# Performance work log

Hardware: AMD Instinct MI355X
Metric: run time of the kernel (lower is better)

Reference implementation:

```python
import jax, jax.numpy as jnp
import numpy as np

TAU = 2.0       # init_tau
VTH = 1.0       # v_threshold
VRESET = 0.0    # v_reset (hard reset)
ALPHA = 2.0     # ATan surrogate width
H = 8           # num_heads
W = 20          # attention_window
TIME_STEP = 2   # config.time_step -> global_scale uses 1000 // time_step


@jax.custom_vjp
def spike(x):
    return (x >= 0.0).astype(x.dtype)

def _spike_fwd(x):
    return (x >= 0.0).astype(x.dtype), x

def _spike_bwd(x, g):
    # ATan surrogate gradient (spikingjelly default)
    sg = (ALPHA / 2.0) / (1.0 + (jnp.pi / 2.0 * ALPHA * x) ** 2)
    return (g * sg,)

spike.defvjp(_spike_fwd, _spike_bwd)


def lif(x_seq):
    """Multi-step LIF, decay_input=False, hard reset. x_seq: [T, ...] -> spikes [T, ...]."""
    def step(v, x):
        h = v - (v - VRESET) / TAU + x          # neuronal charge (decay_input=False)
        s = spike(h - VTH)
        v_new = s * VRESET + (1.0 - s) * h      # hard reset
        return v_new, s
    _, s_seq = jax.lax.scan(step, jnp.zeros_like(x_seq[0]), x_seq)
    return s_seq


def bn(x, gamma, beta, eps=1e-5):
    # BatchNorm1d step_mode='m': stats over (T, B) per channel (training-mode stats)
    mean = x.mean(axis=(0, 1))
    var = x.var(axis=(0, 1))
    return (x - mean) * jax.lax.rsqrt(var + eps) * gamma + beta


def _shift(a, o):
    # a: [B, H, T, D]; out[..., t, :] = a[..., t + o, :], zero outside -> local band
    if o == 0:
        return a
    B_, H_, T_, D_ = a.shape
    z = jnp.zeros((B_, H_, abs(o), D_), a.dtype)
    if o > 0:
        return jnp.concatenate([a[:, :, o:, :], z], axis=2)
    return jnp.concatenate([z, a[:, :, :o, :]], axis=2)


def _forward(x, wq, wk, wv, w_mattn, w_proj, w_dw, w_pw, bn_gamma, bn_beta):
    T, B, C = x.shape
    D = C // H
    local_scale = 1.0 / np.sqrt(D * (2 * W + 1)).astype(np.float32)
    global_scale = 1.0 / np.sqrt(D * (1000 // TIME_STEP)).astype(np.float32)

    # spiking QKV: pointwise conv (kernel 1) + BN + LIF
    q = lif(bn(jnp.einsum('tbc,dc->tbd', x, wq), bn_gamma[0], bn_beta[0]))
    k = lif(bn(jnp.einsum('tbc,dc->tbd', x, wk), bn_gamma[1], bn_beta[1]))
    v = lif(bn(jnp.einsum('tbc,dc->tbd', x, wv), bn_gamma[2], bn_beta[2]))

    heads = lambda a: a.reshape(T, B, H, D).transpose(1, 2, 0, 3)   # [B,H,T,D]
    unheads = lambda a: a.transpose(2, 0, 1, 3).reshape(T, B, C)    # [T,B,C]
    qh, kh, vh = heads(q), heads(k), heads(v)

    # global spiking self-attention (no softmax): (Q K^T) V * global_scale
    attn = jnp.einsum('bhtd,bhsd->bhts', qh, kh)
    g_spk = lif(unheads(jnp.einsum('bhts,bhsd->bhtd', attn, vh) * global_scale))

    # local sliding-window attention over offsets [-W, W] (banded, no [T,T] matrix)
    out_l = jnp.zeros_like(vh)
    for o in range(-W, W + 1):
        s = jnp.einsum('bhtd,bhtd->bht', qh, _shift(kh, o))
        out_l = out_l + s[..., None] * _shift(vh, o)
    l_spk = lif(unheads(out_l * local_scale))

    # depthwise temporal conv branch on V: v_dw -> LIF -> v_pw (1x1 over heads)
    dw = jax.lax.conv_general_dilated(
        vh, w_dw, window_strides=(1, 1), padding=((4, 4), (0, 0)),
        dimension_numbers=('NCHW', 'OIHW', 'NCHW'), feature_group_count=H)
    dw_spk_h = heads(lif(unheads(dw)))
    dw_out = unheads(jnp.einsum('bhtd,gh->bgtd', dw_spk_h, w_pw))

    # merge branches, then mattn conv+BN+LIF and proj conv+BN+LIF
    y0 = lif(g_spk + l_spk + dw_out)
    y1 = lif(bn(jnp.einsum('tbc,dc->tbd', y0, w_mattn), bn_gamma[3], bn_beta[3]))
    out = lif(bn(jnp.einsum('tbc,dc->tbd', y1, w_proj), bn_gamma[4], bn_beta[4]))
    return out


def setup_inputs() -> dict:
    key = jax.random.key(0)
    ks = jax.random.split(key, 10)
    T, B, C = 500, 8, 512
    sc = 0.03
    x = jax.random.normal(ks[0], (T, B, C), jnp.float32)
    wq = jax.random.normal(ks[1], (C, C), jnp.float32) * sc
    wk = jax.random.normal(ks[2], (C, C), jnp.float32) * sc
    wv = jax.random.normal(ks[3], (C, C), jnp.float32) * sc
    w_mattn = jax.random.normal(ks[4], (C, C), jnp.float32) * sc
    w_proj = jax.random.normal(ks[5], (C, C), jnp.float32) * sc
    w_dw = jax.random.normal(ks[6], (H, 1, 9, 1), jnp.float32) * 0.3   # depthwise (9,1)
    w_pw = jax.random.normal(ks[7], (H, H), jnp.float32) * 0.3         # 1x1 over heads
    bn_gamma = jax.random.uniform(ks[8], (5, C), jnp.float32) + 0.5
    bn_beta = jax.random.normal(ks[9], (5, C), jnp.float32) * 0.1
    return {'x': x, 'wq': wq, 'wk': wk, 'wv': wv, 'w_mattn': w_mattn,
            'w_proj': w_proj, 'w_dw': w_dw, 'w_pw': w_pw,
            'bn_gamma': bn_gamma, 'bn_beta': bn_beta}


def reference(x, wq, wk, wv, w_mattn, w_proj, w_dw, w_pw, bn_gamma, bn_beta):
    return _forward(x, wq, wk, wv, w_mattn, w_proj, w_dw, w_pw, bn_gamma, bn_beta)
```

## Files before the change

kernel.cpp:

```cpp
#include <hip/hip_runtime.h>
#include <cmath>

#define TT 500
#define NTOT 2048000
#define WW 20

typedef _Float16 f16x8 __attribute__((ext_vector_type(8)));
typedef _Float16 f16x4 __attribute__((ext_vector_type(4)));
typedef float f32x4 __attribute__((ext_vector_type(4)));

#define C1SC 4.8828125e-4f
#define C2SC 2.384185791015625e-7f

__device__ __forceinline__ void gload16(const _Float16* g, _Float16* l) {
    __builtin_amdgcn_global_load_lds(
        (const __attribute__((address_space(1))) unsigned int*)g,
        (__attribute__((address_space(3))) unsigned int*)l, 16, 0, 0);
}

__global__ __launch_bounds__(256) void prep_split_k(
    const float* __restrict__ x, const float* __restrict__ wq,
    const float* __restrict__ wk, const float* __restrict__ wv,
    const float* __restrict__ wm, const float* __restrict__ wp,
    _Float16* __restrict__ X0, _Float16* __restrict__ X1, _Float16* __restrict__ X2,
    _Float16* __restrict__ Q0, _Float16* __restrict__ Q1, _Float16* __restrict__ Q2,
    _Float16* __restrict__ M0, _Float16* __restrict__ M1, _Float16* __restrict__ M2,
    _Float16* __restrict__ P0, _Float16* __restrict__ P1, _Float16* __restrict__ P2)
{
    int gid = blockIdx.x * 256 + threadIdx.x;
    const float* src;
    _Float16 *d0, *d1, *d2;
    size_t si, di;
    if (gid < 512000) {
        src = x; d0 = X0; d1 = X1; d2 = X2; si = di = (size_t)gid * 4;
    } else if (gid < 708608) {
        int g = gid - 512000;
        int s3 = g >> 16;
        src = (s3 == 0) ? wq : ((s3 == 1) ? wk : wv);
        d0 = Q0; d1 = Q1; d2 = Q2;
        si = (size_t)(g & 65535) * 4;
        di = (size_t)g * 4;
    } else if (gid < 774144) {
        int g = gid - 708608;
        src = wm; d0 = M0; d1 = M1; d2 = M2; si = di = (size_t)g * 4;
    } else {
        int g = gid - 774144;
        src = wp; d0 = P0; d1 = P1; d2 = P2; si = di = (size_t)g * 4;
    }
    float4 v = *(const float4*)(src + si);
    float f[4] = {v.x, v.y, v.z, v.w};
    f16x4 a, b, c;
#pragma unroll
    for (int i = 0; i < 4; ++i) {
        _Float16 h0 = (_Float16)f[i];
        float r1 = f[i] - (float)h0;
        _Float16 h1 = (_Float16)(r1 * 2048.0f);
        float r2 = r1 - (float)h1 * C1SC;
        _Float16 h2 = (_Float16)(r2 * 4194304.0f);
        a[i] = h0; b[i] = h1; c[i] = h2;
    }
    *(f16x4*)(d0 + di) = a;
    *(f16x4*)(d1 + di) = b;
    *(f16x4*)(d2 + di) = c;
}

__global__ __launch_bounds__(256) void gemm_f16s3_k(
    const _Float16* __restrict__ X0, const _Float16* __restrict__ X1,
    const _Float16* __restrict__ X2,
    const _Float16* __restrict__ B0g, const _Float16* __restrict__ B1g,
    const _Float16* __restrict__ B2g,
    float* __restrict__ out, float* __restrict__ colpart, int M)
{
    __shared__ __align__(16) _Float16 sA[18432];
    int tid = threadIdx.x;
    int bid = blockIdx.x;
    int xcd = bid & 7;
    int j = bid >> 3;
    int mblk = (xcd << 3) | (j & 7);
    int nblk = j >> 3;
    int mBase = mblk * 64;
    int nBase = nblk * 128;
    int wv = tid >> 6;
    int lane = tid & 63;
    int wr = wv >> 1, wc = wv & 1;
    int lg = lane >> 4, l16 = lane & 15;

    int subrow = lane >> 2;
    int s4 = lane & 3;
    int rA = (wv << 4) + subrow;
    int sl8 = (s4 ^ ((rA >> 1) & 3)) * 8;
    int mA = mBase + rA; if (mA >= M) mA = 0;
    const _Float16* gA0 = X0 + (size_t)mA * 512 + sl8;
    const _Float16* gA1 = X1 + (size_t)mA * 512 + sl8;
    const _Float16* gA2 = X2 + (size_t)mA * 512 + sl8;
    const _Float16* gB00 = B0g + (size_t)(nBase + rA) * 512 + sl8;
    const _Float16* gB01 = B0g + (size_t)(nBase + 64 + rA) * 512 + sl8;
    const _Float16* gB10 = B1g + (size_t)(nBase + rA) * 512 + sl8;
    const _Float16* gB11 = B1g + (size_t)(nBase + 64 + rA) * 512 + sl8;
    const _Float16* gB20 = B2g + (size_t)(nBase + rA) * 512 + sl8;
    const _Float16* gB21 = B2g + (size_t)(nBase + 64 + rA) * 512 + sl8;
    int wb = wv << 9;
    _Float16* lA0 = sA + wb;
    _Float16* lA1 = sA + 2048 + wb;
    _Float16* lA2 = sA + 4096 + wb;
    _Float16* lB00 = sA + 6144 + wb;
    _Float16* lB01 = sA + 8192 + wb;
    _Float16* lB10 = sA + 10240 + wb;
    _Float16* lB11 = sA + 12288 + wb;
    _Float16* lB20 = sA + 14336 + wb;
    _Float16* lB21 = sA + 16384 + wb;

    int sd = (lg ^ ((l16 >> 1) & 3)) * 8;

    f32x4 acc0[2][4] = {}, acc1[2][4] = {}, acc2[2][4] = {};

    for (int kt = 0; kt < 512; kt += 32) {
        __syncthreads();
        gload16(gA0 + kt, lA0);
        gload16(gA1 + kt, lA1);
        gload16(gA2 + kt, lA2);
        gload16(gB00 + kt, lB00);
        gload16(gB01 + kt, lB01);
        gload16(gB10 + kt, lB10);
        gload16(gB11 + kt, lB11);
        gload16(gB20 + kt, lB20);
        gload16(gB21 + kt, lB21);
        __syncthreads();
        f16x8 a0f[2], a1f[2], a2f[2];
#pragma unroll
        for (int i = 0; i < 2; ++i) {
            int off = (wr * 32 + i * 16 + l16) * 32 + sd;
            a0f[i] = *(const f16x8*)&sA[off];
            a1f[i] = *(const f16x8*)&sA[2048 + off];
            a2f[i] = *(const f16x8*)&sA[4096 + off];
        }
#pragma unroll
        for (int jj = 0; jj < 4; ++jj) {
            int boff = 6144 + (wc * 64 + jj * 16 + l16) * 32 + sd;
            f16x8 b0f = *(const f16x8*)&sA[boff];
            f16x8 b1f = *(const f16x8*)&sA[4096 + boff];
            f16x8 b2f = *(const f16x8*)&sA[8192 + boff];
#pragma unroll
            for (int i = 0; i < 2; ++i) {
                acc0[i][jj] = __builtin_amdgcn_mfma_f32_16x16x32_f16(a0f[i], b0f, acc0[i][jj], 0, 0, 0);
                acc1[i][jj] = __builtin_amdgcn_mfma_f32_16x16x32_f16(a0f[i], b1f, acc1[i][jj], 0, 0, 0);
                acc1[i][jj] = __builtin_amdgcn_mfma_f32_16x16x32_f16(a1f[i], b0f, acc1[i][jj], 0, 0, 0);
                acc2[i][jj] = __builtin_amdgcn_mfma_f32_16x16x32_f16(a1f[i], b1f, acc2[i][jj], 0, 0, 0);
                acc2[i][jj] = __builtin_amdgcn_mfma_f32_16x16x32_f16(a0f[i], b2f, acc2[i][jj], 0, 0, 0);
                acc2[i][jj] = __builtin_amdgcn_mfma_f32_16x16x32_f16(a2f[i], b0f, acc2[i][jj], 0, 0, 0);
            }
        }
    }
#pragma unroll
    for (int i = 0; i < 2; ++i)
#pragma unroll
        for (int jj = 0; jj < 4; ++jj)
#pragma unroll
            for (int r = 0; r < 4; ++r)
                acc0[i][jj][r] = fmaf(C2SC, acc2[i][jj][r],
                                      fmaf(C1SC, acc1[i][jj][r], acc0[i][jj][r]));
    __syncthreads();
    float* red = (float*)sA;
#pragma unroll
    for (int jj = 0; jj < 4; ++jj) {
        float s = 0.f, q = 0.f;
#pragma unroll
        for (int i = 0; i < 2; ++i)
#pragma unroll
            for (int r = 0; r < 4; ++r) {
                int mrow = mBase + wr * 32 + i * 16 + lg * 4 + r;
                float v = (mrow < M) ? acc0[i][jj][r] : 0.f;
                s += v; q = fmaf(v, v, q);
            }
        s += __shfl_xor(s, 16, 64); s += __shfl_xor(s, 32, 64);
        q += __shfl_xor(q, 16, 64); q += __shfl_xor(q, 32, 64);
        if (lane < 16) {
            int col = wc * 64 + jj * 16 + lane;
            red[(wr * 128 + col) * 2 + 0] = s;
            red[(wr * 128 + col) * 2 + 1] = q;
        }
    }
    __syncthreads();
    if (tid < 128) {
        float ss = red[tid * 2 + 0] + red[(128 + tid) * 2 + 0];
        float qq = red[tid * 2 + 1] + red[(128 + tid) * 2 + 1];
        colpart[((size_t)mblk * 1536 + nBase + tid) * 2 + 0] = ss;
        colpart[((size_t)mblk * 1536 + nBase + tid) * 2 + 1] = qq;
    }
    int wsel = nBase >> 9;
    int col0 = nBase & 511;
    float* outp = out + (size_t)wsel * NTOT;
#pragma unroll
    for (int i = 0; i < 2; ++i) {
        int m0 = mBase + wr * 32 + i * 16 + lg * 4;
#pragma unroll
        for (int jj = 0; jj < 4; ++jj) {
            int cc = col0 + wc * 64 + jj * 16 + l16;
#pragma unroll
            for (int r = 0; r < 4; ++r) {
                int m = m0 + r;
                if (m < M) outp[(size_t)m * 512 + cc] = acc0[i][jj][r];
            }
        }
    }
}

__global__ __launch_bounds__(256) void gemm_hs3_k(
    const _Float16* __restrict__ Ah,
    const _Float16* __restrict__ B0g, const _Float16* __restrict__ B1g,
    const _Float16* __restrict__ B2g,
    float* __restrict__ out, float* __restrict__ colpart, int M)
{
    __shared__ __align__(16) _Float16 sH[8192];
    int tid = threadIdx.x;
    int bid = blockIdx.x;
    int xcd = bid & 7;
    int j = bid >> 3;
    int mblk = (xcd << 3) | (j & 7);
    int nblk = j >> 3;
    int mBase = mblk * 64;
    int col0 = nblk * 64;
    int wv = tid >> 6;
    int lane = tid & 63;
    int wr = wv >> 1, wc = wv & 1;
    int lg = lane >> 4, l16 = lane & 15;

    int subrow = lane >> 2;
    int s4 = lane & 3;
    int rA = (wv << 4) + subrow;
    int sl8 = (s4 ^ ((rA >> 1) & 3)) * 8;
    int mA = mBase + rA; if (mA >= M) mA = 0;
    const _Float16* gA  = Ah  + (size_t)mA * 512 + sl8;
    const _Float16* gB0 = B0g + (size_t)(col0 + rA) * 512 + sl8;
    const _Float16* gB1 = B1g + (size_t)(col0 + rA) * 512 + sl8;
    const _Float16* gB2 = B2g + (size_t)(col0 + rA) * 512 + sl8;
    int wb = wv << 9;
    _Float16* lA  = sH + wb;
    _Float16* lB0 = sH + 2048 + wb;
    _Float16* lB1 = sH + 4096 + wb;
    _Float16* lB2 = sH + 6144 + wb;

    int sd = (lg ^ ((l16 >> 1) & 3)) * 8;

    f32x4 acc0[2][2] = {}, acc1[2][2] = {}, acc2[2][2] = {};

    for (int kt = 0; kt < 512; kt += 32) {
        __syncthreads();
        gload16(gA + kt, lA);
        gload16(gB0 + kt, lB0);
        gload16(gB1 + kt, lB1);
        gload16(gB2 + kt, lB2);
        __syncthreads();
        f16x8 af[2];
#pragma unroll
        for (int i = 0; i < 2; ++i)
            af[i] = *(const f16x8*)&sH[(wr * 32 + i * 16 + l16) * 32 + sd];
#pragma unroll
        for (int jj = 0; jj < 2; ++jj) {
            int boff = 2048 + (wc * 32 + jj * 16 + l16) * 32 + sd;
            f16x8 b0f = *(const f16x8*)&sH[boff];
            f16x8 b1f = *(const f16x8*)&sH[2048 + boff];
            f16x8 b2f = *(const f16x8*)&sH[4096 + boff];
#pragma unroll
            for (int i = 0; i < 2; ++i) {
                acc0[i][jj] = __builtin_amdgcn_mfma_f32_16x16x32_f16(af[i], b0f, acc0[i][jj], 0, 0, 0);
                acc1[i][jj] = __builtin_amdgcn_mfma_f32_16x16x32_f16(af[i], b1f, acc1[i][jj], 0, 0, 0);
                acc2[i][jj] = __builtin_amdgcn_mfma_f32_16x16x32_f16(af[i], b2f, acc2[i][jj], 0, 0, 0);
            }
        }
    }
#pragma unroll
    for (int i = 0; i < 2; ++i)
#pragma unroll
        for (int jj = 0; jj < 2; ++jj)
#pragma unroll
            for (int r = 0; r < 4; ++r)
                acc0[i][jj][r] = fmaf(C2SC, acc2[i][jj][r],
                                      fmaf(C1SC, acc1[i][jj][r], acc0[i][jj][r]));
    __syncthreads();
    float* red = (float*)sH;
#pragma unroll
    for (int jj = 0; jj < 2; ++jj) {
        float s = 0.f, q = 0.f;
#pragma unroll
        for (int i = 0; i < 2; ++i)
#pragma unroll
            for (int r = 0; r < 4; ++r) {
                int mrow = mBase + wr * 32 + i * 16 + lg * 4 + r;
                float v = (mrow < M) ? acc0[i][jj][r] : 0.f;
                s += v; q = fmaf(v, v, q);
            }
        s += __shfl_xor(s, 16, 64); s += __shfl_xor(s, 32, 64);
        q += __shfl_xor(q, 16, 64); q += __shfl_xor(q, 32, 64);
        if (lane < 16) {
            int col = wc * 32 + jj * 16 + lane;
            red[(wr * 64 + col) * 2 + 0] = s;
            red[(wr * 64 + col) * 2 + 1] = q;
        }
    }
    __syncthreads();
    if (tid < 64) {
        float ss = red[tid * 2 + 0] + red[(64 + tid) * 2 + 0];
        float qq = red[tid * 2 + 1] + red[(64 + tid) * 2 + 1];
        colpart[((size_t)mblk * 512 + col0 + tid) * 2 + 0] = ss;
        colpart[((size_t)mblk * 512 + col0 + tid) * 2 + 1] = qq;
    }
#pragma unroll
    for (int i = 0; i < 2; ++i) {
        int m0 = mBase + wr * 32 + i * 16 + lg * 4;
#pragma unroll
        for (int jj = 0; jj < 2; ++jj) {
            int cc = col0 + wc * 32 + jj * 16 + l16;
#pragma unroll
            for (int r = 0; r < 4; ++r) {
                int m = m0 + r;
                if (m < M) out[(size_t)m * 512 + cc] = acc0[i][jj][r];
            }
        }
    }
}

__global__ __launch_bounds__(256) void lif_seg_k(
    const float* __restrict__ pre, const float* __restrict__ colpart, int CT, int chunks,
    const float* __restrict__ gamma, const float* __restrict__ beta,
    float* __restrict__ outF, unsigned char* __restrict__ outB,
    _Float16* __restrict__ outH, int segLen, int warm)
{
    int gid = blockIdx.x * 256 + threadIdx.x;
    int tensor = gid >> 12;
    int bc = gid & 4095;
    int ch = (tensor << 9) | (bc & 511);
    double s = 0.0, s2 = 0.0;
    for (int k = 0; k < chunks; ++k) {
        s  += (double)colpart[((size_t)k * CT + ch) * 2 + 0];
        s2 += (double)colpart[((size_t)k * CT + ch) * 2 + 1];
    }
    double mean = s / 4000.0;
    double var = s2 / 4000.0 - mean * mean;
    double scd = (double)gamma[ch] / sqrt(var + 1e-5);
    float sc = (float)scd;
    float sh = (float)((double)beta[ch] - mean * scd);
    const float* q0 = pre + (size_t)tensor * NTOT + bc;
    float* oF = outF ? outF + (size_t)tensor * NTOT + bc : nullptr;
    unsigned char* oB = outB ? outB + (size_t)tensor * NTOT + bc : nullptr;
    _Float16* oH = outH ? outH + (size_t)tensor * NTOT + bc : nullptr;
    int t0 = blockIdx.y * segLen;
    int twarm = (t0 - warm > 0) ? (t0 - warm) : 0;
    int tend = (t0 + segLen < TT) ? (t0 + segLen) : TT;
    float v = 0.f;
    float b0[8];
#pragma unroll
    for (int j = 0; j < 8; ++j) {
        int tt = twarm + j;
        b0[j] = (tt < tend) ? q0[(size_t)tt * 4096] : 0.f;
    }
    for (int t = twarm; t < tend; t += 8) {
        float n0[8];
#pragma unroll
        for (int j = 0; j < 8; ++j) {
            int tt = t + 8 + j;
            n0[j] = (tt < tend) ? q0[(size_t)tt * 4096] : 0.f;
        }
#pragma unroll
        for (int j = 0; j < 8; ++j) {
            int tc = t + j;
            if (tc >= tend) break;
            float bnx = fmaf(b0[j], sc, sh);
            float h = fmaf(0.5f, v, bnx);
            float sp = (h >= 1.f) ? 1.f : 0.f;
            v = (h >= 1.f) ? 0.f : h;
            if (tc >= t0) {
                if (oB)      oB[(size_t)tc * 4096] = (unsigned char)sp;
                else if (oH) oH[(size_t)tc * 4096] = (_Float16)sp;
                else         oF[(size_t)tc * 4096] = sp;
            }
        }
#pragma unroll
        for (int j = 0; j < 8; ++j) b0[j] = n0[j];
    }
}

__global__ __launch_bounds__(256) void ktv_part_k(
    const unsigned char* __restrict__ kspk, const unsigned char* __restrict__ vspk,
    float* __restrict__ part)
{
    __shared__ __align__(16) float kb[16][64], vb[16][64];
    int bh = blockIdx.x;
    int seg = blockIdx.y;
    int t0p = seg * 125, t1p = t0p + 125;
    int b = bh >> 3, h = bh & 7;
    int tid = threadIdx.x;
    int d1b = (tid >> 4) * 4, d2b = (tid & 15) * 4;
    size_t cb = (size_t)b * 512 + h * 64;
    int sRow = tid >> 4;
    int sD = (tid & 15) * 4;
    float acc[4][4] = {};
    uchar4 pk, pv;
    auto preload = [&](int tt) {
        int t = tt + sRow;
        if (t < t1p) {
            pk = *(const uchar4*)(kspk + (size_t)t * 4096 + cb + sD);
            pv = *(const uchar4*)(vspk + (size_t)t * 4096 + cb + sD);
        } else {
            pk = make_uchar4(0, 0, 0, 0); pv = make_uchar4(0, 0, 0, 0);
        }
    };
    preload(t0p);
    for (int tt = t0p; tt < t1p; tt += 16) {
        __syncthreads();
        kb[sRow][sD + 0] = (float)pk.x; kb[sRow][sD + 1] = (float)pk.y;
        kb[sRow][sD + 2] = (float)pk.z; kb[sRow][sD + 3] = (float)pk.w;
        vb[sRow][sD + 0] = (float)pv.x; vb[sRow][sD + 1] = (float)pv.y;
        vb[sRow][sD + 2] = (float)pv.z; vb[sRow][sD + 3] = (float)pv.w;
        __syncthreads();
        preload(tt + 16);
#pragma unroll
        for (int tl = 0; tl < 16; ++tl) {
            float4 k4 = *(const float4*)&kb[tl][d1b];
            float4 v4 = *(const float4*)&vb[tl][d2b];
            float ka[4] = {k4.x, k4.y, k4.z, k4.w};
            float va[4] = {v4.x, v4.y, v4.z, v4.w};
#pragma unroll
            for (int i = 0; i < 4; ++i)
#pragma unroll
                for (int j = 0; j < 4; ++j)
                    acc[i][j] = fmaf(ka[i], va[j], acc[i][j]);
        }
    }
    size_t ob = ((size_t)seg * 64 + bh) * 4096;
#pragma unroll
    for (int i = 0; i < 4; ++i)
        *(float4*)(part + ob + (size_t)(d1b + i) * 64 + d2b) =
            make_float4(acc[i][0], acc[i][1], acc[i][2], acc[i][3]);
}

__global__ __launch_bounds__(256) void ktv_reduce_k(
    const float* __restrict__ part, float* __restrict__ ktv)
{
    int i4 = (blockIdx.x * 256 + threadIdx.x) * 4;
    float4 a = *(const float4*)(part + i4);
    float4 b = *(const float4*)(part + 262144 + i4);
    float4 c = *(const float4*)(part + 2 * 262144 + i4);
    float4 d = *(const float4*)(part + 3 * 262144 + i4);
    *(float4*)(ktv + i4) = make_float4(((a.x + b.x) + c.x) + d.x,
                                       ((a.y + b.y) + c.y) + d.y,
                                       ((a.z + b.z) + c.z) + d.z,
                                       ((a.w + b.w) + c.w) + d.w);
}

__global__ __launch_bounds__(256) void gapply_t_k(
    const unsigned char* __restrict__ sq, const float* __restrict__ ktv,
    float* __restrict__ gpre, float gscale)
{
    __shared__ float qs[10][512];
    int tid = threadIdx.x;
    int t0 = blockIdx.x * 10;
    int b = blockIdx.y;
    for (int i = tid; i < 1280; i += 256) {
        int t = i >> 7;
        int c4 = (i & 127) * 4;
        uchar4 u = *(const uchar4*)(sq + (size_t)(t0 + t) * 4096 + b * 512 + c4);
        qs[t][c4 + 0] = (float)u.x; qs[t][c4 + 1] = (float)u.y;
        qs[t][c4 + 2] = (float)u.z; qs[t][c4 + 3] = (float)u.w;
    }
    __syncthreads();
#pragma unroll
    for (int half = 0; half < 2; ++half) {
        int c = tid + half * 256;
        int h = c >> 6, dcol = c & 63;
        const float* kt = ktv + ((size_t)(b * 8 + h) * 64) * 64 + dcol;
        float acc[10] = {};
        for (int d1 = 0; d1 < 64; ++d1) {
            float kv = kt[(size_t)d1 * 64];
#pragma unroll
            for (int t = 0; t < 10; ++t)
                acc[t] = fmaf(qs[t][h * 64 + d1], kv, acc[t]);
        }
#pragma unroll
        for (int t = 0; t < 10; ++t)
            gpre[(size_t)(t0 + t) * 4096 + b * 512 + c] = acc[t] * gscale;
    }
}

__global__ __launch_bounds__(256) void local_k(
    const unsigned char* __restrict__ qspk, const unsigned char* __restrict__ kspk,
    const unsigned char* __restrict__ vspk, float* __restrict__ lpre, float lscale)
{
    __shared__ __align__(16) float qs[32][68];
    __shared__ __align__(16) float ks[72][68];
    __shared__ __align__(16) float vs[72][68];
    __shared__ float sm[32][72];
    int t0 = blockIdx.x * 32;
    int bh = blockIdx.y;
    int b = bh >> 3, h = bh & 7;
    int tid = threadIdx.x;
    size_t cb = (size_t)b * 512 + h * 64;

    for (int i = tid; i < 512; i += 256) {
        int r = i >> 4, d4 = (i & 15) * 4;
        int t = t0 + r;
        if (t < TT) {
            uchar4 u = *(const uchar4*)(qspk + (size_t)t * 4096 + cb + d4);
            qs[r][d4 + 0] = (float)u.x; qs[r][d4 + 1] = (float)u.y;
            qs[r][d4 + 2] = (float)u.z; qs[r][d4 + 3] = (float)u.w;
        } else {
            qs[r][d4 + 0] = 0.f; qs[r][d4 + 1] = 0.f; qs[r][d4 + 2] = 0.f; qs[r][d4 + 3] = 0.f;
        }
    }
    for (int i = tid; i < 1152; i += 256) {
        int r = i >> 4, d4 = (i & 15) * 4;
        int u_ = t0 - WW + r;
        if (u_ >= 0 && u_ < TT) {
            uchar4 uk = *(const uchar4*)(kspk + (size_t)u_ * 4096 + cb + d4);
            uchar4 uv = *(const uchar4*)(vspk + (size_t)u_ * 4096 + cb + d4);
            ks[r][d4 + 0] = (float)uk.x; ks[r][d4 + 1] = (float)uk.y;
            ks[r][d4 + 2] = (float)uk.z; ks[r][d4 + 3] = (float)uk.w;
            vs[r][d4 + 0] = (float)uv.x; vs[r][d4 + 1] = (float)uv.y;
            vs[r][d4 + 2] = (float)uv.z; vs[r][d4 + 3] = (float)uv.w;
        } else {
            ks[r][d4 + 0] = 0.f; ks[r][d4 + 1] = 0.f; ks[r][d4 + 2] = 0.f; ks[r][d4 + 3] = 0.f;
            vs[r][d4 + 0] = 0.f; vs[r][d4 + 1] = 0.f; vs[r][d4 + 2] = 0.f; vs[r][d4 + 3] = 0.f;
        }
    }
    __syncthreads();

    int tA = tid >> 3;
    int ug = tid & 7;
    float4 qreg[16];
#pragma unroll
    for (int i = 0; i < 16; ++i) qreg[i] = *(const float4*)&qs[tA][i * 4];
#pragma unroll
    for (int ui = 0; ui < 9; ++ui) {
        int u = ug + ui * 8;
        float acc = 0.f;
#pragma unroll
        for (int i = 0; i < 16; ++i) {
            float4 k4 = *(const float4*)&ks[u][i * 4];
            acc = fmaf(qreg[i].x, k4.x, acc);
            acc = fmaf(qreg[i].y, k4.y, acc);
            acc = fmaf(qreg[i].z, k4.z, acc);
            acc = fmaf(qreg[i].w, k4.w, acc);
        }
        sm[tA][u] = acc;
    }
    __syncthreads();

#pragma unroll
    for (int oi = 0; oi < 2; ++oi) {
        int idx = tid + oi * 256;
        int t = idx >> 4;
        int dg = (idx & 15) * 4;
        float4 acc = make_float4(0.f, 0.f, 0.f, 0.f);
        for (int o = 0; o < 41; ++o) {
            int u = t + o;
            float s = sm[t][u];
            float4 v4 = *(const float4*)&vs[u][dg];
            acc.x = fmaf(s, v4.x, acc.x);
            acc.y = fmaf(s, v4.y, acc.y);
            acc.z = fmaf(s, v4.z, acc.z);
            acc.w = fmaf(s, v4.w, acc.w);
        }
        int tg = t0 + t;
        if (tg < TT) {
            acc.x *= lscale; acc.y *= lscale; acc.z *= lscale; acc.w *= lscale;
            *(float4*)(lpre + (size_t)tg * 4096 + cb + dg) = acc;
        }
    }
}

__global__ __launch_bounds__(256) void branch_y0_k(
    const float* __restrict__ gpre, const float* __restrict__ lpre,
    const unsigned char* __restrict__ sv, const float* __restrict__ wdw,
    const float* __restrict__ wpw, _Float16* __restrict__ sy0,
    int segLen, int warm)
{
    int tid = threadIdx.x;
    int wave = tid >> 6, lane = tid & 63;
    int gw = blockIdx.x * 4 + wave;
    int b = gw >> 3, dg = gw & 7;
    int h = lane >> 3, dl = lane & 7;
    int c = h * 64 + dg * 8 + dl;
    int base = b * 512 + c;
    float w9[9];
#pragma unroll
    for (int j = 0; j < 9; ++j) w9[j] = wdw[h * 9 + j];
    float w8[8];
#pragma unroll
    for (int j = 0; j < 8; ++j) w8[j] = wpw[h * 8 + j];
    int t0 = blockIdx.y * segLen;
    int twarm = (t0 - warm > 0) ? (t0 - warm) : 0;
    int tend = (t0 + segLen < TT) ? (t0 + segLen) : TT;
    float vg = 0.f, vl = 0.f, vd = 0.f, vy = 0.f;
    float win[12];
#pragma unroll
    for (int i = 0; i < 12; ++i) {
        int tt = twarm - 4 + i;
        win[i] = (tt >= 0 && tt < TT) ? (float)sv[(size_t)tt * 4096 + base] : 0.f;
    }
    float pg[4], pl[4], pv[4];
    auto pref = [&](int t) {
#pragma unroll
        for (int j = 0; j < 4; ++j) {
            int tt = t + j;
            bool in = tt < tend;
            pg[j] = in ? gpre[(size_t)tt * 4096 + base] : 0.f;
            pl[j] = in ? lpre[(size_t)tt * 4096 + base] : 0.f;
            int tv = t + 8 + j;
            pv[j] = (tv < TT) ? (float)sv[(size_t)tv * 4096 + base] : 0.f;
        }
    };
    pref(twarm);
    for (int t = twarm; t < tend; t += 4) {
        float cg[4], cl[4], cv[4];
#pragma unroll
        for (int j = 0; j < 4; ++j) { cg[j] = pg[j]; cl[j] = pl[j]; cv[j] = pv[j]; }
        pref(t + 4);
#pragma unroll
        for (int j = 0; j < 4; ++j) {
            int tc = t + j;
            if (tc >= tend) break;
            float x = 0.f;
#pragma unroll
            for (int q = 0; q < 9; ++q) x = fmaf(w9[q], win[j + q], x);
            float hd = fmaf(0.5f, vd, x);
            float sd = (hd >= 1.f) ? 1.f : 0.f;
            vd = (hd >= 1.f) ? 0.f : hd;
            float hg = fmaf(0.5f, vg, cg[j]);
            float sg = (hg >= 1.f) ? 1.f : 0.f;
            vg = (hg >= 1.f) ? 0.f : hg;
            float hl = fmaf(0.5f, vl, cl[j]);
            float sl = (hl >= 1.f) ? 1.f : 0.f;
            vl = (hl >= 1.f) ? 0.f : hl;
            float mix = 0.f;
#pragma unroll
            for (int h2 = 0; h2 < 8; ++h2)
                mix = fmaf(w8[h2], __shfl(sd, h2 * 8 + dl, 64), mix);
            float xy = (sg + sl) + mix;
            float hy = fmaf(0.5f, vy, xy);
            float sy = (hy >= 1.f) ? 1.f : 0.f;
            vy = (hy >= 1.f) ? 0.f : hy;
            if (tc >= t0) sy0[(size_t)tc * 4096 + base] = (_Float16)sy;
        }
#pragma unroll
        for (int i = 0; i < 8; ++i) win[i] = win[i + 4];
#pragma unroll
        for (int i = 0; i < 4; ++i) win[8 + i] = cv[i];
    }
}

extern "C" void kernel_launch(void* const* d_in, const int* in_sizes, int n_in,
                              void* d_out, int out_size, void* d_ws, size_t ws_size,
                              hipStream_t stream)
{
    const float* x       = (const float*)d_in[0];
    const float* wq      = (const float*)d_in[1];
    const float* wk      = (const float*)d_in[2];
    const float* wv      = (const float*)d_in[3];
    const float* w_mattn = (const float*)d_in[4];
    const float* w_proj  = (const float*)d_in[5];
    const float* w_dw    = (const float*)d_in[6];
    const float* w_pw    = (const float*)d_in[7];
    const float* bn_g    = (const float*)d_in[8];
    const float* bn_b    = (const float*)d_in[9];
    float* out = (float*)d_out;
    float* ws = (float*)d_ws;

    float gs32 = (float)std::sqrt((double)(64 * 500));
    float gscale = (float)(1.0 / (double)gs32);
    float ls32 = (float)std::sqrt((double)(64 * 41));
    float lscale = (float)(1.0 / (double)ls32);
    const int M = TT * 8;

    float* S0 = ws;
    float* S1 = ws + (size_t)NTOT;
    float* S2 = ws + 2 * (size_t)NTOT;
    float* part4   = ws + 3 * (size_t)NTOT;
    float* ktvBuf  = part4 + 4 * 262144;
    float* colpart = ktvBuf + 262144;
    unsigned char* spk = (unsigned char*)(colpart + 196608);
    unsigned char* sq  = spk;
    unsigned char* sk  = spk + (size_t)NTOT;
    unsigned char* sv  = spk + 2 * (size_t)NTOT;
    _Float16* sy0h = (_Float16*)(spk + 3 * (size_t)NTOT);
    _Float16* sy1h = (_Float16*)spk;
    _Float16* X0 = (_Float16*)spk;
    _Float16* X1 = X0 + (size_t)NTOT;
    _Float16* X2 = X1 + (size_t)NTOT;
    _Float16* Wm0 = (_Float16*)(spk + 6 * (size_t)NTOT);
    _Float16* Wm1 = Wm0 + 262144;
    _Float16* Wm2 = Wm1 + 262144;
    _Float16* Wp0 = Wm2 + 262144;
    _Float16* Wp1 = Wp0 + 262144;
    _Float16* Wp2 = Wp1 + 262144;
    _Float16* Wq0 = (_Float16*)part4;
    _Float16* Wq1 = Wq0 + 786432;
    _Float16* Wq2 = Wq1 + 786432;

    prep_split_k<<<3280, 256, 0, stream>>>(x, wq, wk, wv, w_mattn, w_proj,
                                           X0, X1, X2, Wq0, Wq1, Wq2,
                                           Wm0, Wm1, Wm2, Wp0, Wp1, Wp2);
    gemm_f16s3_k<<<768, 256, 0, stream>>>(X0, X1, X2, Wq0, Wq1, Wq2, S0, colpart, M);
    lif_seg_k<<<dim3(48, 10), 256, 0, stream>>>(S0, colpart, 1536, 64, bn_g, bn_b,
                                                nullptr, sq, nullptr, 50, 64);
    ktv_part_k<<<dim3(64, 4), 256, 0, stream>>>(sk, sv, part4);
    ktv_reduce_k<<<256, 256, 0, stream>>>(part4, ktvBuf);
    gapply_t_k<<<dim3(50, 8), 256, 0, stream>>>(sq, ktvBuf, S0, gscale);
    local_k<<<dim3(16, 64), 256, 0, stream>>>(sq, sk, sv, S1, lscale);
    branch_y0_k<<<dim3(16, 20), 256, 0, stream>>>(S0, S1, sv, w_dw, w_pw, sy0h, 25, 64);
    gemm_hs3_k<<<512, 256, 0, stream>>>(sy0h, Wm0, Wm1, Wm2, S2, colpart, M);
    lif_seg_k<<<dim3(16, 20), 256, 0, stream>>>(S2, colpart, 512, 64, bn_g + 1536,
                                                bn_b + 1536, nullptr, nullptr, sy1h, 25, 64);
    gemm_hs3_k<<<512, 256, 0, stream>>>(sy1h, Wp0, Wp1, Wp2, S0, colpart, M);
    lif_seg_k<<<dim3(16, 20), 256, 0, stream>>>(S0, colpart, 512, 64, bn_g + 2048,
                                                bn_b + 2048, out, nullptr, nullptr, 25, 64);

    (void)in_sizes; (void)n_in; (void)out_size; (void)ws_size;
}
```

Measured before the change: 341.6 us.

## Double-buffer LDS tiles in split-f16 GEMM kernels to overlap loads with MFMA

Both split-precision GEMM kernels now keep two LDS buffers and issue the global-to-LDS loads for the next K tile before computing on the current one, with one barrier per iteration instead of two. This is meant to hide global load latency behind the MFMA work. LDS use per block doubles (about 72KB in the first kernel), which may cut occupancy. Correctness relies on the barrier making the async LDS loads visible before the buffer is read.

```diff
diff --git a/kernel.cpp b/kernel.cpp
--- a/kernel.cpp
+++ b/kernel.cpp
@@ -71,7 +71,7 @@
     const _Float16* __restrict__ B2g,
     float* __restrict__ out, float* __restrict__ colpart, int M)
 {
-    __shared__ __align__(16) _Float16 sA[18432];
+    __shared__ __align__(16) _Float16 sA[36864];
     int tid = threadIdx.x;
     int bid = blockIdx.x;
     int xcd = bid & 7;
@@ -110,33 +110,39 @@
     _Float16* lB20 = sA + 14336 + wb;
     _Float16* lB21 = sA + 16384 + wb;
 
+    auto stage = [&](int kt, int off) {
+        gload16(gA0 + kt, lA0 + off);
+        gload16(gA1 + kt, lA1 + off);
+        gload16(gA2 + kt, lA2 + off);
+        gload16(gB00 + kt, lB00 + off);
+        gload16(gB01 + kt, lB01 + off);
+        gload16(gB10 + kt, lB10 + off);
+        gload16(gB11 + kt, lB11 + off);
+        gload16(gB20 + kt, lB20 + off);
+        gload16(gB21 + kt, lB21 + off);
+    };
+
     int sd = (lg ^ ((l16 >> 1) & 3)) * 8;
 
     f32x4 acc0[2][4] = {}, acc1[2][4] = {}, acc2[2][4] = {};
 
+    stage(0, 0);
+    __syncthreads();
+    int cur = 0;
     for (int kt = 0; kt < 512; kt += 32) {
-        __syncthreads();
-        gload16(gA0 + kt, lA0);
-        gload16(gA1 + kt, lA1);
-        gload16(gA2 + kt, lA2);
-        gload16(gB00 + kt, lB00);
-        gload16(gB01 + kt, lB01);
-        gload16(gB10 + kt, lB10);
-        gload16(gB11 + kt, lB11);
-        gload16(gB20 + kt, lB20);
-        gload16(gB21 + kt, lB21);
-        __syncthreads();
+        int coff = cur * 18432;
+        if (kt + 32 < 512) stage(kt + 32, 18432 - coff);
         f16x8 a0f[2], a1f[2], a2f[2];
 #pragma unroll
         for (int i = 0; i < 2; ++i) {
-            int off = (wr * 32 + i * 16 + l16) * 32 + sd;
+            int off = (wr * 32 + i * 16 + l16) * 32 + sd + coff;
             a0f[i] = *(const f16x8*)&sA[off];
             a1f[i] = *(const f16x8*)&sA[2048 + off];
             a2f[i] = *(const f16x8*)&sA[4096 + off];
         }
 #pragma unroll
         for (int jj = 0; jj < 4; ++jj) {
-            int boff = 6144 + (wc * 64 + jj * 16 + l16) * 32 + sd;
+            int boff = 6144 + (wc * 64 + jj * 16 + l16) * 32 + sd + coff;
             f16x8 b0f = *(const f16x8*)&sA[boff];
             f16x8 b1f = *(const f16x8*)&sA[4096 + boff];
             f16x8 b2f = *(const f16x8*)&sA[8192 + boff];
@@ -150,6 +156,8 @@
                 acc2[i][jj] = __builtin_amdgcn_mfma_f32_16x16x32_f16(a2f[i], b0f, acc2[i][jj], 0, 0, 0);
             }
         }
+        __syncthreads();
+        cur ^= 1;
     }
 #pragma unroll
     for (int i = 0; i < 2; ++i)
@@ -159,7 +167,6 @@
             for (int r = 0; r < 4; ++r)
                 acc0[i][jj][r] = fmaf(C2SC, acc2[i][jj][r],
                                       fmaf(C1SC, acc1[i][jj][r], acc0[i][jj][r]));
-    __syncthreads();
     float* red = (float*)sA;
 #pragma unroll
     for (int jj = 0; jj < 4; ++jj) {
@@ -211,7 +218,7 @@
     const _Float16* __restrict__ B2g,
     float* __restrict__ out, float* __restrict__ colpart, int M)
 {
-    __shared__ __align__(16) _Float16 sH[8192];
+    __shared__ __align__(16) _Float16 sH[16384];
     int tid = threadIdx.x;
     int bid = blockIdx.x;
     int xcd = bid & 7;
@@ -240,24 +247,30 @@
     _Float16* lB1 = sH + 4096 + wb;
     _Float16* lB2 = sH + 6144 + wb;
 
+    auto stage = [&](int kt, int off) {
+        gload16(gA + kt, lA + off);
+        gload16(gB0 + kt, lB0 + off);
+        gload16(gB1 + kt, lB1 + off);
+        gload16(gB2 + kt, lB2 + off);
+    };
+
     int sd = (lg ^ ((l16 >> 1) & 3)) * 8;
 
     f32x4 acc0[2][2] = {}, acc1[2][2] = {}, acc2[2][2] = {};
 
+    stage(0, 0);
+    __syncthreads();
+    int cur = 0;
     for (int kt = 0; kt < 512; kt += 32) {
-        __syncthreads();
-        gload16(gA + kt, lA);
-        gload16(gB0 + kt, lB0);
-        gload16(gB1 + kt, lB1);
-        gload16(gB2 + kt, lB2);
-        __syncthreads();
+        int coff = cur * 8192;
+        if (kt + 32 < 512) stage(kt + 32, 8192 - coff);
         f16x8 af[2];
 #pragma unroll
         for (int i = 0; i < 2; ++i)
-            af[i] = *(const f16x8*)&sH[(wr * 32 + i * 16 + l16) * 32 + sd];
+            af[i] = *(const f16x8*)&sH[(wr * 32 + i * 16 + l16) * 32 + sd + coff];
 #pragma unroll
         for (int jj = 0; jj < 2; ++jj) {
-            int boff = 2048 + (wc * 32 + jj * 16 + l16) * 32 + sd;
+            int boff = 2048 + (wc * 32 + jj * 16 + l16) * 32 + sd + coff;
             f16x8 b0f = *(const f16x8*)&sH[boff];
             f16x8 b1f = *(const f16x8*)&sH[2048 + boff];
             f16x8 b2f = *(const f16x8*)&sH[4096 + boff];
@@ -268,6 +281,8 @@
                 acc2[i][jj] = __builtin_amdgcn_mfma_f32_16x16x32_f16(af[i], b2f, acc2[i][jj], 0, 0, 0);
             }
         }
+        __syncthreads();
+        cur ^= 1;
     }
 #pragma unroll
     for (int i = 0; i < 2; ++i)
@@ -277,7 +292,6 @@
             for (int r = 0; r < 4; ++r)
                 acc0[i][jj][r] = fmaf(C2SC, acc2[i][jj][r],
                                       fmaf(C1SC, acc1[i][jj][r], acc0[i][jj][r]));
-    __syncthreads();
     float* red = (float*)sH;
 #pragma unroll
     for (int jj = 0; jj < 2; ++jj) {
```

Result: faster. 331.7 us (-2.9%).
